# Performance work log

Hardware: AMD Instinct MI355X
Metric: run time of the kernel (lower is better)

The kernel has to match this reference:

```python
import jax, jax.numpy as jnp
import numpy as np

DG = 8   # deformable_groups
KK = 9   # 3x3 kernel
NEG_SLOPE = 0.2


def conv3x3(x, w, b):
    y = jax.lax.conv_general_dilated(x, w, (1, 1), ((1, 1), (1, 1)),
                                     dimension_numbers=('NCHW', 'OIHW', 'NCHW'))
    return y + b[None, :, None, None]


def deform_sample(x, oy, ox, mask):
    # x: [B,C,H,W]; oy/ox/mask: [B,DG,KK,H,W] -> sampled [B,DG,cpg,KK,H,W]
    B, C, H, W = x.shape
    cpg = C // DG
    ky, kx = jnp.meshgrid(jnp.arange(3), jnp.arange(3), indexing='ij')
    ky = (ky.reshape(-1) - 1).astype(x.dtype)  # dilation=1, padding=1
    kx = (kx.reshape(-1) - 1).astype(x.dtype)
    hh = jnp.arange(H, dtype=x.dtype)
    ww = jnp.arange(W, dtype=x.dtype)
    py = hh[None, None, None, :, None] + ky[None, None, :, None, None] + oy
    px = ww[None, None, None, None, :] + kx[None, None, :, None, None] + ox
    y0 = jnp.floor(py)
    x0 = jnp.floor(px)
    fy = py - y0
    fx = px - x0
    xg = x.reshape(B, DG, cpg, H * W)

    def gather(yi, xi):
        valid = ((yi >= 0) & (yi < H) & (xi >= 0) & (xi < W)).astype(x.dtype)
        yc = jnp.clip(yi, 0, H - 1)
        xc = jnp.clip(xi, 0, W - 1)
        idx = (yc * W + xc).reshape(B, DG, 1, KK * H * W)
        v = jnp.take_along_axis(xg, idx, axis=3).reshape(B, DG, cpg, KK, H, W)
        return v * valid[:, :, None]

    y0i = y0.astype(jnp.int32)
    x0i = x0.astype(jnp.int32)
    v00 = gather(y0i, x0i)
    v01 = gather(y0i, x0i + 1)
    v10 = gather(y0i + 1, x0i)
    v11 = gather(y0i + 1, x0i + 1)
    wy = fy[:, :, None]
    wx = fx[:, :, None]
    val = (v00 * (1 - wy) * (1 - wx) + v01 * (1 - wy) * wx
           + v10 * wy * (1 - wx) + v11 * wy * wx)
    return val * mask[:, :, None]


def reference(x, offset, w_off, b_off, w_dcn, b_dcn, w_conv1, b_conv1):
    B, C, H, W = x.shape
    om = conv3x3(offset, w_off, b_off)  # [B, 3*DG*KK, H, W]
    o1, o2, m = jnp.split(om, 3, axis=1)
    oy = o1.reshape(B, DG, KK, H, W)
    ox = o2.reshape(B, DG, KK, H, W)
    mask = jax.nn.sigmoid(m).reshape(B, DG, KK, H, W)
    sampled = deform_sample(x, oy, ox, mask)  # [B,DG,cpg,KK,H,W]
    wd = w_dcn.reshape(w_dcn.shape[0], DG, C // DG, KK)
    dcn = jnp.einsum('bgckhw,ogck->bohw', sampled, wd) + b_dcn[None, :, None, None]
    fea = jnp.where(dcn >= 0, dcn, NEG_SLOPE * dcn)  # LeakyReLU(0.2)
    out = conv3x3(fea, w_conv1, b_conv1) + x  # residual
    return out


def setup_inputs() -> dict:
    key = jax.random.key(0)
    ks = jax.random.split(key, 8)
    B, C, H, W = 4, 64, 96, 96
    offC = 64
    s = 1.0 / np.sqrt(C * 9)
    return {
        'x': jax.random.normal(ks[0], (B, C, H, W), jnp.float32),
        'offset': jax.random.normal(ks[1], (B, offC, H, W), jnp.float32),
        'w_off': jax.random.normal(ks[2], (3 * DG * KK, offC, 3, 3), jnp.float32) * 0.05,
        'b_off': jnp.zeros((3 * DG * KK,), jnp.float32),
        'w_dcn': jax.random.normal(ks[3], (C, C, 3, 3), jnp.float32) * s,
        'b_dcn': jnp.zeros((C,), jnp.float32),
        'w_conv1': jax.random.normal(ks[4], (C, C, 3, 3), jnp.float32) * s,
        'b_conv1': jnp.zeros((C,), jnp.float32),
    }
```

## Files before the change

kernel.cpp:

```cpp
#include <hip/hip_runtime.h>
#include <math.h>

#define HH 96
#define WW 96
#define NB 4
#define NC 64
#define HW (HH*WW)

typedef unsigned short u16;
typedef unsigned int   u32;
typedef __attribute__((ext_vector_type(8))) short bf16x8;
typedef __attribute__((ext_vector_type(4))) float f32x4;

__device__ inline float bf2f(u16 v) { u32 u = ((u32)v) << 16; return __uint_as_float(u); }
__device__ inline u16 f2bf(float f) {
    u32 u = __float_as_uint(f);
    return (u16)((u + 0x7FFFu + ((u >> 16) & 1u)) >> 16);
}

__global__ __launch_bounds__(256) void k_nhwc2(
    const float* __restrict__ s0, const float* __restrict__ s1,
    u16* __restrict__ d0, u16* __restrict__ d1) {
    const float* src = blockIdx.y ? s1 : s0;
    u16* dst = blockIdx.y ? d1 : d0;
    int pix = blockIdx.x * 256 + threadIdx.x;
    int b = pix / HW, hw = pix % HW;
    const float* s = src + b * 64 * HW + hw;
    uint4* dp = (uint4*)(dst + pix * 64);
#pragma unroll
    for (int q = 0; q < 8; ++q) {
        u32 a0 = (u32)f2bf(s[(q*8+0)*HW]) | ((u32)f2bf(s[(q*8+1)*HW]) << 16);
        u32 a1 = (u32)f2bf(s[(q*8+2)*HW]) | ((u32)f2bf(s[(q*8+3)*HW]) << 16);
        u32 a2 = (u32)f2bf(s[(q*8+4)*HW]) | ((u32)f2bf(s[(q*8+5)*HW]) << 16);
        u32 a3 = (u32)f2bf(s[(q*8+6)*HW]) | ((u32)f2bf(s[(q*8+7)*HW]) << 16);
        dp[q] = make_uint4(a0, a1, a2, a3);
    }
}

__global__ void k_wtb3(const float* __restrict__ w_off, const float* __restrict__ w_dcn,
                       const float* __restrict__ w_c1, u16* __restrict__ d_off,
                       u16* __restrict__ d_dcn, u16* __restrict__ d_c1) {
    int m = blockIdx.y;
    const float* w = (m == 0) ? w_off : ((m == 1) ? w_dcn : w_c1);
    u16* dst = (m == 0) ? d_off : ((m == 1) ? d_dcn : d_c1);
    int NT   = (m == 0) ? 14 : 4;
    int NCO  = (m == 0) ? 216 : 64;
    int mode = (m == 1) ? 0 : 1;
    int n = 18 * NT * 512;
    int i = blockIdx.x * 256 + threadIdx.x;
    if (i >= n) return;
    int j = i & 7, L = (i >> 3) & 63;
    int cot = (i >> 9) % NT, t = (i >> 9) / NT;
    int k = t * 32 + ((L >> 4) << 3) + j;
    int co = cot * 16 + (L & 15);
    float v = 0.f;
    if (co < NCO) {
        int ci, q;
        if (mode == 0) { int c = k & 7, gk = k >> 3; int kk = gk % 9, g = gk / 9; ci = g*8+c; q = kk; }
        else           { q = k >> 6; ci = k & 63; }
        v = w[co * 576 + ci * 9 + q];
    }
    dst[i] = f2bf(v);
}

__global__ __launch_bounds__(256) void k_gemm_off(
    const u16* __restrict__ ot, const u16* __restrict__ wtb,
    const float* __restrict__ bias, u16* __restrict__ om) {
    __shared__ u16 lb[7168];
    int tid = threadIdx.x;
    int wid = tid >> 6, L = tid & 63, lr = L & 15, lk = L >> 4;
    int pixbase = blockIdx.x * 64 + wid * 16;
    int pixA = pixbase + lr;
    int b = pixbase / HW;
    int hw = pixA % HW, y = hw / WW, x = hw % WW;

    f32x4 acc[14];
#pragma unroll
    for (int i = 0; i < 14; ++i) acc[i] = (f32x4){0.f, 0.f, 0.f, 0.f};

    for (int t = 0; t < 18; ++t) {
        if (t) __syncthreads();
        {
            const uint4* s = (const uint4*)(wtb + t * 7168);
            uint4* d = (uint4*)lb;
            for (int i = tid; i < 896; i += 256) d[i] = s[i];
        }
        __syncthreads();
        int q = t >> 1;
        int c0 = (t & 1) * 32 + lk * 8;
        int dy = q / 3 - 1, dx = q % 3 - 1;
        int yy = y + dy, xx = x + dx;
        bf16x8 a = {0,0,0,0,0,0,0,0};
        if (yy >= 0 && yy < HH && xx >= 0 && xx < WW)
            a = *(const bf16x8*)(ot + ((b * HH + yy) * WW + xx) * 64 + c0);
        const u16* wp = lb + L * 8;
#pragma unroll
        for (int cot = 0; cot < 14; ++cot) {
            bf16x8 bf = *(const bf16x8*)(wp + cot * 512);
            acc[cot] = __builtin_amdgcn_mfma_f32_16x16x32_bf16(a, bf, acc[cot], 0, 0, 0);
        }
    }
    int pixC = pixbase + lk * 4;
#pragma unroll
    for (int cot = 0; cot < 14; ++cot) {
        int co = cot * 16 + lr;
        if (co < 216) {
#pragma unroll
            for (int r = 0; r < 4; ++r) {
                float v = acc[cot][r] + bias[co];
                om[(pixC + r) * 216 + co] = f2bf(v);
            }
        }
    }
}

__device__ __forceinline__ void sample4(
    const u16* __restrict__ xt, const u16* __restrict__ om,
    u16* __restrict__ sv, int pix, int p, int b, int h, int w, int ga) {
    const u16* omp = om + pix * 216 + ga * 9;
    const u16* xb  = xt + b * HW * 64 + ga * 8;
    int gl = ga & 3;
#pragma unroll
    for (int kk = 0; kk < 9; ++kk) {
        float oy = bf2f(omp[kk]);
        float ox = bf2f(omp[72 + kk]);
        float mv = bf2f(omp[144 + kk]);
        float mask = 1.f / (1.f + __expf(-mv));

        float py = (float)(h + kk / 3 - 1) + oy;
        float px = (float)(w + kk % 3 - 1) + ox;
        float y0f = floorf(py), x0f = floorf(px);
        float fy = py - y0f, fx = px - x0f;
        int y0 = (int)y0f, x0 = (int)x0f, y1 = y0 + 1, x1 = x0 + 1;
        int yc0 = min(max(y0, 0), HH-1), yc1 = min(max(y1, 0), HH-1);
        int xc0 = min(max(x0, 0), WW-1), xc1 = min(max(x1, 0), WW-1);
        float u0 = 1.f - fy, u1 = fy, s0 = 1.f - fx, s1 = fx;
        float w00 = (y0 >= 0 && y0 < HH && x0 >= 0 && x0 < WW) ? u0*s0*mask : 0.f;
        float w01 = (y0 >= 0 && y0 < HH && x1 >= 0 && x1 < WW) ? u0*s1*mask : 0.f;
        float w10 = (y1 >= 0 && y1 < HH && x0 >= 0 && x0 < WW) ? u1*s0*mask : 0.f;
        float w11 = (y1 >= 0 && y1 < HH && x1 >= 0 && x1 < WW) ? u1*s1*mask : 0.f;

        uint4 q00 = *(const uint4*)(xb + (yc0*WW + xc0)*64);
        uint4 q01 = *(const uint4*)(xb + (yc0*WW + xc1)*64);
        uint4 q10 = *(const uint4*)(xb + (yc1*WW + xc0)*64);
        uint4 q11 = *(const uint4*)(xb + (yc1*WW + xc1)*64);

        float r[8];
        {
            float a, bb, c, d;
            a=__uint_as_float(q00.x<<16); bb=__uint_as_float(q01.x<<16); c=__uint_as_float(q10.x<<16); d=__uint_as_float(q11.x<<16);
            r[0]=w00*a+w01*bb+w10*c+w11*d;
            a=__uint_as_float(q00.x&0xFFFF0000u); bb=__uint_as_float(q01.x&0xFFFF0000u); c=__uint_as_float(q10.x&0xFFFF0000u); d=__uint_as_float(q11.x&0xFFFF0000u);
            r[1]=w00*a+w01*bb+w10*c+w11*d;
            a=__uint_as_float(q00.y<<16); bb=__uint_as_float(q01.y<<16); c=__uint_as_float(q10.y<<16); d=__uint_as_float(q11.y<<16);
            r[2]=w00*a+w01*bb+w10*c+w11*d;
            a=__uint_as_float(q00.y&0xFFFF0000u); bb=__uint_as_float(q01.y&0xFFFF0000u); c=__uint_as_float(q10.y&0xFFFF0000u); d=__uint_as_float(q11.y&0xFFFF0000u);
            r[3]=w00*a+w01*bb+w10*c+w11*d;
            a=__uint_as_float(q00.z<<16); bb=__uint_as_float(q01.z<<16); c=__uint_as_float(q10.z<<16); d=__uint_as_float(q11.z<<16);
            r[4]=w00*a+w01*bb+w10*c+w11*d;
            a=__uint_as_float(q00.z&0xFFFF0000u); bb=__uint_as_float(q01.z&0xFFFF0000u); c=__uint_as_float(q10.z&0xFFFF0000u); d=__uint_as_float(q11.z&0xFFFF0000u);
            r[5]=w00*a+w01*bb+w10*c+w11*d;
            a=__uint_as_float(q00.w<<16); bb=__uint_as_float(q01.w<<16); c=__uint_as_float(q10.w<<16); d=__uint_as_float(q11.w<<16);
            r[6]=w00*a+w01*bb+w10*c+w11*d;
            a=__uint_as_float(q00.w&0xFFFF0000u); bb=__uint_as_float(q01.w&0xFFFF0000u); c=__uint_as_float(q10.w&0xFFFF0000u); d=__uint_as_float(q11.w&0xFFFF0000u);
            r[7]=w00*a+w01*bb+w10*c+w11*d;
        }
        u32 a0 = (u32)f2bf(r[0]) | ((u32)f2bf(r[1]) << 16);
        u32 a1 = (u32)f2bf(r[2]) | ((u32)f2bf(r[3]) << 16);
        u32 a2 = (u32)f2bf(r[4]) | ((u32)f2bf(r[5]) << 16);
        u32 a3 = (u32)f2bf(r[6]) | ((u32)f2bf(r[7]) << 16);
        int slot = gl * 9 + kk;
        *(uint4*)((char*)sv + p * 640 + ((slot * 16) ^ ((p & 7) << 4))) = make_uint4(a0, a1, a2, a3);
    }
}

__global__ __launch_bounds__(256) void k_sdcn(
    const u16* __restrict__ xt, const u16* __restrict__ om,
    const u16* __restrict__ wtb, const float* __restrict__ bias,
    u16* __restrict__ fea) {
    __shared__ u16 sv[64 * 320];
    int tid = threadIdx.x;
    int pixblk = blockIdx.x * 64;
    int p = tid >> 2, g = tid & 3;
    int pix = pixblk + p;
    int b = pix / HW, hw = pix % HW, h = hw / WW, w = hw % WW;
    int wid = tid >> 6, L = tid & 63, lr = L & 15, lk = L >> 4;
    int prow = wid * 16 + lr;

    f32x4 acc[4];
#pragma unroll
    for (int i = 0; i < 4; ++i) acc[i] = (f32x4){0.f, 0.f, 0.f, 0.f};

    sample4(xt, om, sv, pix, p, b, h, w, g);
    __syncthreads();
#pragma unroll
    for (int tl = 0; tl < 9; ++tl) {
        bf16x8 a = *(const bf16x8*)((const char*)sv + prow * 640 + (((tl * 4 + lk) * 16) ^ ((prow & 7) << 4)));
        const u16* wp = wtb + (tl * 256 + L) * 8;
#pragma unroll
        for (int cot = 0; cot < 4; ++cot) {
            bf16x8 bf = *(const bf16x8*)(wp + cot * 512);
            acc[cot] = __builtin_amdgcn_mfma_f32_16x16x32_bf16(a, bf, acc[cot], 0, 0, 0);
        }
    }
    __syncthreads();
    sample4(xt, om, sv, pix, p, b, h, w, g + 4);
    __syncthreads();
#pragma unroll
    for (int tl = 0; tl < 9; ++tl) {
        bf16x8 a = *(const bf16x8*)((const char*)sv + prow * 640 + (((tl * 4 + lk) * 16) ^ ((prow & 7) << 4)));
        const u16* wp = wtb + ((tl + 9) * 256 + L) * 8;
#pragma unroll
        for (int cot = 0; cot < 4; ++cot) {
            bf16x8 bf = *(const bf16x8*)(wp + cot * 512);
            acc[cot] = __builtin_amdgcn_mfma_f32_16x16x32_bf16(a, bf, acc[cot], 0, 0, 0);
        }
    }
    int pixC = pixblk + wid * 16 + lk * 4;
#pragma unroll
    for (int cot = 0; cot < 4; ++cot) {
        int co = cot * 16 + lr;
#pragma unroll
        for (int r = 0; r < 4; ++r) {
            float v = acc[cot][r] + bias[co];
            v = (v >= 0.f) ? v : 0.2f * v;
            fea[(pixC + r) * 64 + co] = f2bf(v);
        }
    }
}

__global__ __launch_bounds__(256) void k_gemm_c1(
    const u16* __restrict__ fea, const u16* __restrict__ wtb,
    const float* __restrict__ bias, const float* __restrict__ xres,
    float* __restrict__ out) {
    __shared__ __align__(16) char smraw[36864];
    u16* lb = (u16*)smraw;
    int tid = threadIdx.x;
    int wid = tid >> 6, L = tid & 63, lr = L & 15, lk = L >> 4;
    int pixblk = blockIdx.x * 64;
    int pixbase = pixblk + wid * 16;
    int pixA = pixbase + lr;
    int b = pixblk / HW;
    int hw = pixA % HW, y = hw / WW, x = hw % WW;

    f32x4 acc[4];
#pragma unroll
    for (int i = 0; i < 4; ++i) acc[i] = (f32x4){0.f, 0.f, 0.f, 0.f};

    {
        const uint4* s = (const uint4*)wtb;
        uint4* d = (uint4*)lb;
#pragma unroll
        for (int i = 0; i < 9; ++i) d[tid + i * 256] = s[tid + i * 256];
    }
    __syncthreads();
    for (int half = 0; half < 2; ++half) {
        int tbase = half * 9;
#pragma unroll
        for (int tl = 0; tl < 9; ++tl) {
            int t = tbase + tl;
            int q = t >> 1;
            int c0 = (t & 1) * 32 + lk * 8;
            int dy = q / 3 - 1, dx = q % 3 - 1;
            int yy = y + dy, xx = x + dx;
            bf16x8 a = {0,0,0,0,0,0,0,0};
            if (yy >= 0 && yy < HH && xx >= 0 && xx < WW)
                a = *(const bf16x8*)(fea + ((b * HH + yy) * WW + xx) * 64 + c0);
            const u16* wp = lb + (tl * 256 + L) * 8;
#pragma unroll
            for (int cot = 0; cot < 4; ++cot) {
                bf16x8 bf = *(const bf16x8*)(wp + cot * 512);
                acc[cot] = __builtin_amdgcn_mfma_f32_16x16x32_bf16(a, bf, acc[cot], 0, 0, 0);
            }
        }
        __syncthreads();
        if (half == 0) {
            const uint4* s = (const uint4*)(wtb + 18432);
            uint4* d = (uint4*)lb;
#pragma unroll
            for (int i = 0; i < 9; ++i) d[tid + i * 256] = s[tid + i * 256];
            __syncthreads();
        }
    }
    float* ob = (float*)smraw;
#pragma unroll
    for (int cot = 0; cot < 4; ++cot) {
#pragma unroll
        for (int r = 0; r < 4; ++r)
            ob[(wid * 16 + lk * 4 + r) * 66 + cot * 16 + lr] = acc[cot][r];
    }
    __syncthreads();
    int p = tid & 63, cg = tid >> 6;
    int hw0 = pixblk % HW;
#pragma unroll
    for (int i = 0; i < 16; ++i) {
        int co = cg * 16 + i;
        int idx = (b * 64 + co) * HW + hw0 + p;
        out[idx] = ob[p * 66 + co] + bias[co] + xres[idx];
    }
}

extern "C" void kernel_launch(void* const* d_in, const int* in_sizes, int n_in,
                              void* d_out, int out_size, void* d_ws, size_t ws_size,
                              hipStream_t stream) {
    const float* x       = (const float*)d_in[0];
    const float* offset  = (const float*)d_in[1];
    const float* w_off   = (const float*)d_in[2];
    const float* b_off   = (const float*)d_in[3];
    const float* w_dcn   = (const float*)d_in[4];
    const float* b_dcn   = (const float*)d_in[5];
    const float* w_conv1 = (const float*)d_in[6];
    const float* b_conv1 = (const float*)d_in[7];
    float* out = (float*)d_out;

    char* ws = (char*)d_ws;
    u16* om      = (u16*)(ws);
    u16* xt      = (u16*)(ws + 15925248);
    u16* ot      = (u16*)(ws + 20643840);
    u16* fea     = (u16*)(ws + 25362432);
    u16* wtb_off = (u16*)(ws + 30081024);
    u16* wtb_dcn = (u16*)(ws + 30339072);
    u16* wtb_c1  = (u16*)(ws + 30412800);

    hipLaunchKernelGGL(k_nhwc2, dim3(144, 2), dim3(256), 0, stream, x, offset, xt, ot);
    hipLaunchKernelGGL(k_wtb3, dim3(504, 3), dim3(256), 0, stream,
                       w_off, w_dcn, w_conv1, wtb_off, wtb_dcn, wtb_c1);
    hipLaunchKernelGGL(k_gemm_off, dim3(576), dim3(256), 0, stream, ot, wtb_off, b_off, om);
    hipLaunchKernelGGL(k_sdcn, dim3(576), dim3(256), 0, stream, xt, om, wtb_dcn, b_dcn, fea);
    hipLaunchKernelGGL(k_gemm_c1, dim3(576), dim3(256), 0, stream, fea, wtb_c1, b_conv1, x, out);
}
```

Before: 177.4 us.

## Merge prep kernels, regroup offset/mask layout, sigmoid in GEMM epilogue, restructure sampling

Fuses the NHWC conversion and weight-packing kernels into one launch, and exact-sizes the weight blocks. The offset GEMM now applies the mask sigmoid in its epilogue and writes a 256-wide per-pixel record grouped by deformable group, so each sampling thread fetches its 27 values with four 16-byte loads. The deformable kernel now handles 32 pixels per block with 8 threads per pixel, so all groups are sampled in one pass with a single barrier. The waves split the output channels for the MFMA reduction. The cost is a larger intermediate buffer and twice as many sdcn blocks.

```diff
diff --git a/kernel.cpp b/kernel.cpp
--- a/kernel.cpp
+++ b/kernel.cpp
@@ -17,38 +17,48 @@
     u32 u = __float_as_uint(f);
     return (u16)((u + 0x7FFFu + ((u >> 16) & 1u)) >> 16);
 }
-
-__global__ __launch_bounds__(256) void k_nhwc2(
-    const float* __restrict__ s0, const float* __restrict__ s1,
-    u16* __restrict__ d0, u16* __restrict__ d1) {
-    const float* src = blockIdx.y ? s1 : s0;
-    u16* dst = blockIdx.y ? d1 : d0;
-    int pix = blockIdx.x * 256 + threadIdx.x;
-    int b = pix / HW, hw = pix % HW;
-    const float* s = src + b * 64 * HW + hw;
-    uint4* dp = (uint4*)(dst + pix * 64);
-#pragma unroll
-    for (int q = 0; q < 8; ++q) {
-        u32 a0 = (u32)f2bf(s[(q*8+0)*HW]) | ((u32)f2bf(s[(q*8+1)*HW]) << 16);
-        u32 a1 = (u32)f2bf(s[(q*8+2)*HW]) | ((u32)f2bf(s[(q*8+3)*HW]) << 16);
-        u32 a2 = (u32)f2bf(s[(q*8+4)*HW]) | ((u32)f2bf(s[(q*8+5)*HW]) << 16);
-        u32 a3 = (u32)f2bf(s[(q*8+6)*HW]) | ((u32)f2bf(s[(q*8+7)*HW]) << 16);
-        dp[q] = make_uint4(a0, a1, a2, a3);
-    }
-}
-
-__global__ void k_wtb3(const float* __restrict__ w_off, const float* __restrict__ w_dcn,
-                       const float* __restrict__ w_c1, u16* __restrict__ d_off,
-                       u16* __restrict__ d_dcn, u16* __restrict__ d_c1) {
-    int m = blockIdx.y;
+__device__ __forceinline__ float elemf(const u32* a, int i) {
+    u32 v = a[i >> 1];
+    v = (i & 1) ? (v & 0xFFFF0000u) : (v << 16);
+    return __uint_as_float(v);
+}
+
+__global__ __launch_bounds__(256) void k_prep(
+    const float* __restrict__ x, const float* __restrict__ offset,
+    const float* __restrict__ w_off, const float* __restrict__ w_dcn,
+    const float* __restrict__ w_c1,
+    u16* __restrict__ xt, u16* __restrict__ ot,
+    u16* __restrict__ d_off, u16* __restrict__ d_dcn, u16* __restrict__ d_c1) {
+    int bx = blockIdx.x;
+    int tid = threadIdx.x;
+    if (bx < 288) {
+        const float* src = (bx < 144) ? x : offset;
+        u16* dst = (bx < 144) ? xt : ot;
+        int pix = (bx % 144) * 256 + tid;
+        int b = pix / HW, hw = pix % HW;
+        const float* s = src + b * 64 * HW + hw;
+        uint4* dp = (uint4*)(dst + pix * 64);
+#pragma unroll
+        for (int q = 0; q < 8; ++q) {
+            u32 a0 = (u32)f2bf(s[(q*8+0)*HW]) | ((u32)f2bf(s[(q*8+1)*HW]) << 16);
+            u32 a1 = (u32)f2bf(s[(q*8+2)*HW]) | ((u32)f2bf(s[(q*8+3)*HW]) << 16);
+            u32 a2 = (u32)f2bf(s[(q*8+4)*HW]) | ((u32)f2bf(s[(q*8+5)*HW]) << 16);
+            u32 a3 = (u32)f2bf(s[(q*8+6)*HW]) | ((u32)f2bf(s[(q*8+7)*HW]) << 16);
+            dp[q] = make_uint4(a0, a1, a2, a3);
+        }
+        return;
+    }
+    int rel = bx - 288;
+    int m, i0;
+    if (rel < 504)      { m = 0; i0 = rel * 256; }
+    else if (rel < 648) { m = 1; i0 = (rel - 504) * 256; }
+    else                { m = 2; i0 = (rel - 648) * 256; }
     const float* w = (m == 0) ? w_off : ((m == 1) ? w_dcn : w_c1);
     u16* dst = (m == 0) ? d_off : ((m == 1) ? d_dcn : d_c1);
     int NT   = (m == 0) ? 14 : 4;
     int NCO  = (m == 0) ? 216 : 64;
-    int mode = (m == 1) ? 0 : 1;
-    int n = 18 * NT * 512;
-    int i = blockIdx.x * 256 + threadIdx.x;
-    if (i >= n) return;
+    int i = i0 + tid;
+    if (i >= 18 * NT * 512) return;
     int j = i & 7, L = (i >> 3) & 63;
     int cot = (i >> 9) % NT, t = (i >> 9) / NT;
     int k = t * 32 + ((L >> 4) << 3) + j;
@@ -56,8 +66,8 @@
     float v = 0.f;
     if (co < NCO) {
         int ci, q;
-        if (mode == 0) { int c = k & 7, gk = k >> 3; int kk = gk % 9, g = gk / 9; ci = g*8+c; q = kk; }
-        else           { q = k >> 6; ci = k & 63; }
+        if (m == 1) { int c = k & 7, gk = k >> 3; int kk = gk % 9, g = gk / 9; ci = g*8+c; q = kk; }
+        else        { q = k >> 6; ci = k & 63; }
         v = w[co * 576 + ci * 9 + q];
     }
     dst[i] = f2bf(v);
@@ -65,7 +75,7 @@
 
 __global__ __launch_bounds__(256) void k_gemm_off(
     const u16* __restrict__ ot, const u16* __restrict__ wtb,
-    const float* __restrict__ bias, u16* __restrict__ om) {
+    const float* __restrict__ bias, u16* __restrict__ omr) {
     __shared__ u16 lb[7168];
     int tid = threadIdx.x;
     int wid = tid >> 6, L = tid & 63, lr = L & 15, lk = L >> 4;
@@ -105,126 +115,117 @@
     for (int cot = 0; cot < 14; ++cot) {
         int co = cot * 16 + lr;
         if (co < 216) {
+            int cls = co / 72;
+            int c   = co % 72;
+            int g   = c / 9, kk = c % 9;
+            int slot = g * 32 + cls * 9 + kk;
 #pragma unroll
             for (int r = 0; r < 4; ++r) {
                 float v = acc[cot][r] + bias[co];
-                om[(pixC + r) * 216 + co] = f2bf(v);
+                if (cls == 2) v = 1.f / (1.f + __expf(-v));
+                omr[(pixC + r) * 256 + slot] = f2bf(v);
             }
         }
     }
 }
 
-__device__ __forceinline__ void sample4(
-    const u16* __restrict__ xt, const u16* __restrict__ om,
-    u16* __restrict__ sv, int pix, int p, int b, int h, int w, int ga) {
-    const u16* omp = om + pix * 216 + ga * 9;
-    const u16* xb  = xt + b * HW * 64 + ga * 8;
-    int gl = ga & 3;
-#pragma unroll
-    for (int kk = 0; kk < 9; ++kk) {
-        float oy = bf2f(omp[kk]);
-        float ox = bf2f(omp[72 + kk]);
-        float mv = bf2f(omp[144 + kk]);
-        float mask = 1.f / (1.f + __expf(-mv));
-
-        float py = (float)(h + kk / 3 - 1) + oy;
-        float px = (float)(w + kk % 3 - 1) + ox;
-        float y0f = floorf(py), x0f = floorf(px);
-        float fy = py - y0f, fx = px - x0f;
-        int y0 = (int)y0f, x0 = (int)x0f, y1 = y0 + 1, x1 = x0 + 1;
-        int yc0 = min(max(y0, 0), HH-1), yc1 = min(max(y1, 0), HH-1);
-        int xc0 = min(max(x0, 0), WW-1), xc1 = min(max(x1, 0), WW-1);
-        float u0 = 1.f - fy, u1 = fy, s0 = 1.f - fx, s1 = fx;
-        float w00 = (y0 >= 0 && y0 < HH && x0 >= 0 && x0 < WW) ? u0*s0*mask : 0.f;
-        float w01 = (y0 >= 0 && y0 < HH && x1 >= 0 && x1 < WW) ? u0*s1*mask : 0.f;
-        float w10 = (y1 >= 0 && y1 < HH && x0 >= 0 && x0 < WW) ? u1*s0*mask : 0.f;
-        float w11 = (y1 >= 0 && y1 < HH && x1 >= 0 && x1 < WW) ? u1*s1*mask : 0.f;
-
-        uint4 q00 = *(const uint4*)(xb + (yc0*WW + xc0)*64);
-        uint4 q01 = *(const uint4*)(xb + (yc0*WW + xc1)*64);
-        uint4 q10 = *(const uint4*)(xb + (yc1*WW + xc0)*64);
-        uint4 q11 = *(const uint4*)(xb + (yc1*WW + xc1)*64);
-
-        float r[8];
-        {
-            float a, bb, c, d;
-            a=__uint_as_float(q00.x<<16); bb=__uint_as_float(q01.x<<16); c=__uint_as_float(q10.x<<16); d=__uint_as_float(q11.x<<16);
-            r[0]=w00*a+w01*bb+w10*c+w11*d;
-            a=__uint_as_float(q00.x&0xFFFF0000u); bb=__uint_as_float(q01.x&0xFFFF0000u); c=__uint_as_float(q10.x&0xFFFF0000u); d=__uint_as_float(q11.x&0xFFFF0000u);
-            r[1]=w00*a+w01*bb+w10*c+w11*d;
-            a=__uint_as_float(q00.y<<16); bb=__uint_as_float(q01.y<<16); c=__uint_as_float(q10.y<<16); d=__uint_as_float(q11.y<<16);
-            r[2]=w00*a+w01*bb+w10*c+w11*d;
-            a=__uint_as_float(q00.y&0xFFFF0000u); bb=__uint_as_float(q01.y&0xFFFF0000u); c=__uint_as_float(q10.y&0xFFFF0000u); d=__uint_as_float(q11.y&0xFFFF0000u);
-            r[3]=w00*a+w01*bb+w10*c+w11*d;
-            a=__uint_as_float(q00.z<<16); bb=__uint_as_float(q01.z<<16); c=__uint_as_float(q10.z<<16); d=__uint_as_float(q11.z<<16);
-            r[4]=w00*a+w01*bb+w10*c+w11*d;
-            a=__uint_as_float(q00.z&0xFFFF0000u); bb=__uint_as_float(q01.z&0xFFFF0000u); c=__uint_as_float(q10.z&0xFFFF0000u); d=__uint_as_float(q11.z&0xFFFF0000u);
-            r[5]=w00*a+w01*bb+w10*c+w11*d;
-            a=__uint_as_float(q00.w<<16); bb=__uint_as_float(q01.w<<16); c=__uint_as_float(q10.w<<16); d=__uint_as_float(q11.w<<16);
-            r[6]=w00*a+w01*bb+w10*c+w11*d;
-            a=__uint_as_float(q00.w&0xFFFF0000u); bb=__uint_as_float(q01.w&0xFFFF0000u); c=__uint_as_float(q10.w&0xFFFF0000u); d=__uint_as_float(q11.w&0xFFFF0000u);
-            r[7]=w00*a+w01*bb+w10*c+w11*d;
-        }
-        u32 a0 = (u32)f2bf(r[0]) | ((u32)f2bf(r[1]) << 16);
-        u32 a1 = (u32)f2bf(r[2]) | ((u32)f2bf(r[3]) << 16);
-        u32 a2 = (u32)f2bf(r[4]) | ((u32)f2bf(r[5]) << 16);
-        u32 a3 = (u32)f2bf(r[6]) | ((u32)f2bf(r[7]) << 16);
-        int slot = gl * 9 + kk;
-        *(uint4*)((char*)sv + p * 640 + ((slot * 16) ^ ((p & 7) << 4))) = make_uint4(a0, a1, a2, a3);
-    }
-}
-
 __global__ __launch_bounds__(256) void k_sdcn(
-    const u16* __restrict__ xt, const u16* __restrict__ om,
+    const u16* __restrict__ xt, const u16* __restrict__ omr,
     const u16* __restrict__ wtb, const float* __restrict__ bias,
     u16* __restrict__ fea) {
-    __shared__ u16 sv[64 * 320];
+    __shared__ u16 sv[32 * 576];
     int tid = threadIdx.x;
-    int pixblk = blockIdx.x * 64;
-    int p = tid >> 2, g = tid & 3;
+    int pixblk = blockIdx.x * 32;
+    int p = tid >> 3, g = tid & 7;
     int pix = pixblk + p;
-    int b = pix / HW, hw = pix % HW, h = hw / WW, w = hw % WW;
+    int b = pixblk / HW;
+    int hw = pix % HW, h = hw / WW, w = hw % WW;
+
+    {
+        const u16* xb = xt + b * HW * 64 + g * 8;
+        const uint4* op = (const uint4*)(omr + (size_t)pix * 256 + g * 32);
+        uint4 o0 = op[0], o1 = op[1], o2 = op[2], o3 = op[3];
+        u32 oa[16] = {o0.x,o0.y,o0.z,o0.w, o1.x,o1.y,o1.z,o1.w,
+                      o2.x,o2.y,o2.z,o2.w, o3.x,o3.y,o3.z,o3.w};
+#pragma unroll
+        for (int kk = 0; kk < 9; ++kk) {
+            float oy   = elemf(oa, kk);
+            float ox   = elemf(oa, 9 + kk);
+            float mask = elemf(oa, 18 + kk);
+
+            float py = (float)(h + kk / 3 - 1) + oy;
+            float px = (float)(w + kk % 3 - 1) + ox;
+            float y0f = floorf(py), x0f = floorf(px);
+            float fy = py - y0f, fx = px - x0f;
+            int y0 = (int)y0f, x0 = (int)x0f, y1 = y0 + 1, x1 = x0 + 1;
+            int yc0 = min(max(y0, 0), HH-1), yc1 = min(max(y1, 0), HH-1);
+            int xc0 = min(max(x0, 0), WW-1), xc1 = min(max(x1, 0), WW-1);
+            float u0 = 1.f - fy, u1 = fy, s0 = 1.f - fx, s1 = fx;
+            float w00 = (y0 >= 0 && y0 < HH && x0 >= 0 && x0 < WW) ? u0*s0*mask : 0.f;
+            float w01 = (y0 >= 0 && y0 < HH && x1 >= 0 && x1 < WW) ? u0*s1*mask : 0.f;
+            float w10 = (y1 >= 0 && y1 < HH && x0 >= 0 && x0 < WW) ? u1*s0*mask : 0.f;
+            float w11 = (y1 >= 0 && y1 < HH && x1 >= 0 && x1 < WW) ? u1*s1*mask : 0.f;
+
+            uint4 q00 = *(const uint4*)(xb + (yc0*WW + xc0)*64);
+            uint4 q01 = *(const uint4*)(xb + (yc0*WW + xc1)*64);
+            uint4 q10 = *(const uint4*)(xb + (yc1*WW + xc0)*64);
+            uint4 q11 = *(const uint4*)(xb + (yc1*WW + xc1)*64);
+
+            float r[8];
+            {
+                float a, bb, c, d;
+                a=__uint_as_float(q00.x<<16); bb=__uint_as_float(q01.x<<16); c=__uint_as_float(q10.x<<16); d=__uint_as_float(q11.x<<16);
+                r[0]=w00*a+w01*bb+w10*c+w11*d;
+                a=__uint_as_float(q00.x&0xFFFF0000u); bb=__uint_as_float(q01.x&0xFFFF0000u); c=__uint_as_float(q10.x&0xFFFF0000u); d=__uint_as_float(q11.x&0xFFFF0000u);
+                r[1]=w00*a+w01*bb+w10*c+w11*d;
+                a=__uint_as_float(q00.y<<16); bb=__uint_as_float(q01.y<<16); c=__uint_as_float(q10.y<<16); d=__uint_as_float(q11.y<<16);
+                r[2]=w00*a+w01*bb+w10*c+w11*d;
+                a=__uint_as_float(q00.y&0xFFFF0000u); bb=__uint_as_float(q01.y&0xFFFF0000u); c=__uint_as_float(q10.y&0xFFFF0000u); d=__uint_as_float(q11.y&0xFFFF0000u);
+                r[3]=w00*a+w01*bb+w10*c+w11*d;
+                a=__uint_as_float(q00.z<<16); bb=__uint_as_float(q01.z<<16); c=__uint_as_float(q10.z<<16); d=__uint_as_float(q11.z<<16);
+                r[4]=w00*a+w01*bb+w10*c+w11*d;
+                a=__uint_as_float(q00.z&0xFFFF0000u); bb=__uint_as_float(q01.z&0xFFFF0000u); c=__uint_as_float(q10.z&0xFFFF0000u); d=__uint_as_float(q11.z&0xFFFF0000u);
+                r[5]=w00*a+w01*bb+w10*c+w11*d;
+                a=__uint_as_float(q00.w<<16); bb=__uint_as_float(q01.w<<16); c=__uint_as_float(q10.w<<16); d=__uint_as_float(q11.w<<16);
+                r[6]=w00*a+w01*bb+w10*c+w11*d;
+                a=__uint_as_float(q00.w&0xFFFF0000u); bb=__uint_as_float(q01.w&0xFFFF0000u); c=__uint_as_float(q10.w&0xFFFF0000u); d=__uint_as_float(q11.w&0xFFFF0000u);
+                r[7]=w00*a+w01*bb+w10*c+w11*d;
+            }
+            u32 a0 = (u32)f2bf(r[0]) | ((u32)f2bf(r[1]) << 16);
+            u32 a1 = (u32)f2bf(r[2]) | ((u32)f2bf(r[3]) << 16);
+            u32 a2 = (u32)f2bf(r[4]) | ((u32)f2bf(r[5]) << 16);
+            u32 a3 = (u32)f2bf(r[6]) | ((u32)f2bf(r[7]) << 16);
+            int slot = g * 9 + kk;
+            *(uint4*)((char*)sv + p * 1152 + ((slot * 16) ^ ((p & 7) << 4))) = make_uint4(a0, a1, a2, a3);
+        }
+    }
+    __syncthreads();
+
     int wid = tid >> 6, L = tid & 63, lr = L & 15, lk = L >> 4;
-    int prow = wid * 16 + lr;
-
-    f32x4 acc[4];
-#pragma unroll
-    for (int i = 0; i < 4; ++i) acc[i] = (f32x4){0.f, 0.f, 0.f, 0.f};
-
-    sample4(xt, om, sv, pix, p, b, h, w, g);
-    __syncthreads();
-#pragma unroll
-    for (int tl = 0; tl < 9; ++tl) {
-        bf16x8 a = *(const bf16x8*)((const char*)sv + prow * 640 + (((tl * 4 + lk) * 16) ^ ((prow & 7) << 4)));
-        const u16* wp = wtb + (tl * 256 + L) * 8;
-#pragma unroll
-        for (int cot = 0; cot < 4; ++cot) {
-            bf16x8 bf = *(const bf16x8*)(wp + cot * 512);
-            acc[cot] = __builtin_amdgcn_mfma_f32_16x16x32_bf16(a, bf, acc[cot], 0, 0, 0);
-        }
-    }
-    __syncthreads();
-    sample4(xt, om, sv, pix, p, b, h, w, g + 4);
-    __syncthreads();
-#pragma unroll
-    for (int tl = 0; tl < 9; ++tl) {
-        bf16x8 a = *(const bf16x8*)((const char*)sv + prow * 640 + (((tl * 4 + lk) * 16) ^ ((prow & 7) << 4)));
-        const u16* wp = wtb + ((tl + 9) * 256 + L) * 8;
-#pragma unroll
-        for (int cot = 0; cot < 4; ++cot) {
-            bf16x8 bf = *(const bf16x8*)(wp + cot * 512);
-            acc[cot] = __builtin_amdgcn_mfma_f32_16x16x32_bf16(a, bf, acc[cot], 0, 0, 0);
-        }
-    }
-    int pixC = pixblk + wid * 16 + lk * 4;
-#pragma unroll
-    for (int cot = 0; cot < 4; ++cot) {
-        int co = cot * 16 + lr;
+    int pbase = (wid & 1) * 16, cbase = (wid >> 1) * 2;
+    int arow = pbase + lr;
+
+    f32x4 acc[2];
+    acc[0] = (f32x4){0.f, 0.f, 0.f, 0.f};
+    acc[1] = (f32x4){0.f, 0.f, 0.f, 0.f};
+#pragma unroll
+    for (int t = 0; t < 18; ++t) {
+        bf16x8 a = *(const bf16x8*)((const char*)sv + arow * 1152 + (((t * 4 + lk) * 16) ^ ((arow & 7) << 4)));
+#pragma unroll
+        for (int ct = 0; ct < 2; ++ct) {
+            bf16x8 bf = *(const bf16x8*)(wtb + ((t * 4 + cbase + ct) * 64 + L) * 8);
+            acc[ct] = __builtin_amdgcn_mfma_f32_16x16x32_bf16(a, bf, acc[ct], 0, 0, 0);
+        }
+    }
+#pragma unroll
+    for (int ct = 0; ct < 2; ++ct) {
+        int co = (cbase + ct) * 16 + lr;
+        float bs = bias[co];
 #pragma unroll
         for (int r = 0; r < 4; ++r) {
-            float v = acc[cot][r] + bias[co];
+            float v = acc[ct][r] + bs;
             v = (v >= 0.f) ? v : 0.2f * v;
-            fea[(pixC + r) * 64 + co] = f2bf(v);
+            fea[(pixblk + pbase + lk * 4 + r) * 64 + co] = f2bf(v);
         }
     }
 }
@@ -314,18 +315,17 @@
     float* out = (float*)d_out;
 
     char* ws = (char*)d_ws;
-    u16* om      = (u16*)(ws);
-    u16* xt      = (u16*)(ws + 15925248);
-    u16* ot      = (u16*)(ws + 20643840);
-    u16* fea     = (u16*)(ws + 25362432);
-    u16* wtb_off = (u16*)(ws + 30081024);
-    u16* wtb_dcn = (u16*)(ws + 30339072);
-    u16* wtb_c1  = (u16*)(ws + 30412800);
-
-    hipLaunchKernelGGL(k_nhwc2, dim3(144, 2), dim3(256), 0, stream, x, offset, xt, ot);
-    hipLaunchKernelGGL(k_wtb3, dim3(504, 3), dim3(256), 0, stream,
-                       w_off, w_dcn, w_conv1, wtb_off, wtb_dcn, wtb_c1);
-    hipLaunchKernelGGL(k_gemm_off, dim3(576), dim3(256), 0, stream, ot, wtb_off, b_off, om);
-    hipLaunchKernelGGL(k_sdcn, dim3(576), dim3(256), 0, stream, xt, om, wtb_dcn, b_dcn, fea);
+    u16* omr     = (u16*)(ws);
+    u16* xt      = (u16*)(ws + 18874368);
+    u16* ot      = (u16*)(ws + 23592960);
+    u16* fea     = (u16*)(ws + 28311552);
+    u16* wtb_off = (u16*)(ws + 33030144);
+    u16* wtb_dcn = (u16*)(ws + 33288192);
+    u16* wtb_c1  = (u16*)(ws + 33361920);
+
+    hipLaunchKernelGGL(k_prep, dim3(1080), dim3(256), 0, stream,
+                       x, offset, w_off, w_dcn, w_conv1, xt, ot, wtb_off, wtb_dcn, wtb_c1);
+    hipLaunchKernelGGL(k_gemm_off, dim3(576), dim3(256), 0, stream, ot, wtb_off, b_off, omr);
+    hipLaunchKernelGGL(k_sdcn, dim3(1152), dim3(256), 0, stream, xt, omr, wtb_dcn, b_dcn, fea);
     hipLaunchKernelGGL(k_gemm_c1, dim3(576), dim3(256), 0, stream, fea, wtb_c1, b_conv1, x, out);
 }
```

After: 164.9 us. 7.1% less time.
